# Optimization experiments

Hardware: AMD Instinct MI355X
Metric: run time of the kernel (lower is better)

Reference implementation:

```python
import jax, jax.numpy as jnp
import numpy as np

D_MODEL = 512
N_HEADS = 8
D_KV = 64
EPS = 1e-6
ROPE_THETA = 10000.0


def _rms_norm(x, w):
    # T5-style RMSNorm: no mean subtraction, no bias, variance in fp32.
    var = jnp.mean(x.astype(jnp.float32) ** 2, axis=-1, keepdims=True)
    return (x * jax.lax.rsqrt(var + EPS)).astype(x.dtype) * w


def _rope_cos_sin(pos, dk):
    # pos: [B, T] int -> cos/sin: [B, 1, T, dk]
    inv_freq = 1.0 / (ROPE_THETA ** (jnp.arange(0, dk, 2, dtype=jnp.float32) / dk))
    ang = pos.astype(jnp.float32)[:, :, None] * inv_freq[None, None, :]  # [B,T,dk/2]
    ang = jnp.concatenate([ang, ang], axis=-1)                            # [B,T,dk]
    return jnp.cos(ang)[:, None], jnp.sin(ang)[:, None]


def _rotate_half(x):
    h = x.shape[-1] // 2
    return jnp.concatenate([-x[..., h:], x[..., :h]], axis=-1)


def _mha(x, mask, wq, wk, wv, wo, pos=None):
    # x: [B, T, D]; mask: [B, H, T, T] additive
    B, T, _ = x.shape
    def proj(w):
        return (x @ w).reshape(B, T, N_HEADS, D_KV).transpose(0, 2, 1, 3)  # [B,H,T,dk]
    q, k, v = proj(wq), proj(wk), proj(wv)
    if pos is not None:
        cos, sin = _rope_cos_sin(pos, D_KV)
        cos, sin = cos.astype(x.dtype), sin.astype(x.dtype)
        q = q * cos + _rotate_half(q) * sin
        k = k * cos + _rotate_half(k) * sin
    scale = 1.0 / np.sqrt(D_KV)
    scores = jnp.einsum('bhqd,bhkd->bhqk', q, k) * scale + mask
    attn = jax.nn.softmax(scores.astype(jnp.float32), axis=-1).astype(scores.dtype)
    out = jnp.einsum('bhqk,bhkd->bhqd', attn, v)
    out = out.transpose(0, 2, 1, 3).reshape(B, T, N_HEADS * D_KV)
    return out @ wo


def setup_inputs() -> dict:
    key = jax.random.key(0)
    ks = jax.random.split(key, 12)
    B, T = 8, 1024
    s = 1.0 / np.sqrt(D_MODEL)
    inp = {
        'h': jax.random.normal(ks[0], (B, T, D_MODEL), dtype=jnp.float32),
        'pos': jnp.broadcast_to(jnp.arange(T, dtype=jnp.int64 if jax.config.jax_enable_x64 else jnp.int32)[None, :], (B, T)),
        't_mask': jnp.zeros((B, N_HEADS, T, T), dtype=jnp.float32),
        'g_mask': jnp.zeros((T, N_HEADS, B, B), dtype=jnp.float32),
        'ln_t_w': jnp.ones((D_MODEL,), dtype=jnp.float32),
        'ln_g_w': jnp.ones((D_MODEL,), dtype=jnp.float32),
    }
    names = ['wq_t', 'wk_t', 'wv_t', 'wo_t', 'wq_g', 'wk_g', 'wv_g', 'wo_g']
    for i, n in enumerate(names):
        inp[n] = jax.random.normal(ks[i + 1], (D_MODEL, D_MODEL), dtype=jnp.float32) * s
    return inp


def reference(h, pos, t_mask, g_mask, ln_t_w, ln_g_w,
              wq_t, wk_t, wv_t, wo_t, wq_g, wk_g, wv_g, wo_g):
    # --- time attention (over T axis, with RoPE) ---
    normed = _rms_norm(h, ln_t_w)
    attn_t = _mha(normed, t_mask, wq_t, wk_t, wv_t, wo_t, pos=pos)
    h = h + attn_t  # dropout p=0 (eval)
    # --- group attention (over B axis, no RoPE) ---
    h = h.transpose(1, 0, 2)  # [T, B, D]
    normed = _rms_norm(h, ln_g_w)
    attn_g = _mha(normed, g_mask, wq_g, wk_g, wv_g, wo_g, pos=None)
    h = h + attn_g
    return h.transpose(1, 0, 2)  # back to [B, T, D]
```

## Files before the change

### kernel.cpp

```cpp
#include <hip/hip_runtime.h>
#include <hip/hip_bf16.h>
#include <math.h>


typedef __bf16 bf16x8 __attribute__((ext_vector_type(8)));
typedef __bf16 bf16x4 __attribute__((ext_vector_type(4)));
typedef float  f32x4  __attribute__((ext_vector_type(4)));

#define LN1E4_OVER_32 0.2878231366242558f

__global__ __launch_bounds__(256) void transpose_w(
    const float* w0, const float* w1, const float* w2, const float* w3,
    const float* w4, const float* w5, const float* w6, const float* w7,
    __bf16* qkvT_t, __bf16* oT_t, __bf16* qkvT_g, __bf16* oT_g)
{
    int mat = blockIdx.z;
    const float* src; __bf16* dst; int rowOff;
    switch (mat) {
        case 0: src=w0; dst=qkvT_t; rowOff=0;    break;
        case 1: src=w1; dst=qkvT_t; rowOff=512;  break;
        case 2: src=w2; dst=qkvT_t; rowOff=1024; break;
        case 3: src=w3; dst=oT_t;   rowOff=0;    break;
        case 4: src=w4; dst=qkvT_g; rowOff=0;    break;
        case 5: src=w5; dst=qkvT_g; rowOff=512;  break;
        case 6: src=w6; dst=qkvT_g; rowOff=1024; break;
        default: src=w7; dst=oT_g;  rowOff=0;    break;
    }
    __shared__ float tile[32][33];
    int n0 = blockIdx.x * 32, k0 = blockIdx.y * 32;
    int tt = threadIdx.x;
    int kr = tt >> 3, nc = (tt & 7) * 4;
    float4 v = *(const float4*)(src + (size_t)(k0 + kr) * 512 + n0 + nc);
    tile[kr][nc+0] = v.x; tile[kr][nc+1] = v.y; tile[kr][nc+2] = v.z; tile[kr][nc+3] = v.w;
    __syncthreads();
    int nr = tt >> 3, kc = (tt & 7) * 4;
    bf16x4 o;
    o[0] = (__bf16)tile[kc+0][nr]; o[1] = (__bf16)tile[kc+1][nr];
    o[2] = (__bf16)tile[kc+2][nr]; o[3] = (__bf16)tile[kc+3][nr];
    *(bf16x4*)(dst + (size_t)(rowOff + n0 + nr) * 512 + k0 + kc) = o;
}

__global__ __launch_bounds__(256) void rmsnorm_k(
    const float* __restrict__ x, const float* __restrict__ w,
    __bf16* __restrict__ y, int remap)
{
    int row = blockIdx.x * 4 + (threadIdx.x >> 6);
    int l = threadIdx.x & 63;
    const float* xr = x + (size_t)row * 512 + l * 8;
    float4 a = *(const float4*)xr;
    float4 b = *(const float4*)(xr + 4);
    float ss = a.x*a.x + a.y*a.y + a.z*a.z + a.w*a.w
             + b.x*b.x + b.y*b.y + b.z*b.z + b.w*b.w;
    for (int m = 1; m < 64; m <<= 1) ss += __shfl_xor(ss, m);
    float rms = rsqrtf(ss * (1.0f / 512.0f) + 1e-6f);
    float4 wa = *(const float4*)(w + l * 8);
    float4 wb = *(const float4*)(w + l * 8 + 4);
    int orow = remap ? ((row & 1023) * 8 + (row >> 10)) : row;
    bf16x8 o;
    o[0] = (__bf16)(a.x * rms * wa.x); o[1] = (__bf16)(a.y * rms * wa.y);
    o[2] = (__bf16)(a.z * rms * wa.z); o[3] = (__bf16)(a.w * rms * wa.w);
    o[4] = (__bf16)(b.x * rms * wb.x); o[5] = (__bf16)(b.y * rms * wb.y);
    o[6] = (__bf16)(b.z * rms * wb.z); o[7] = (__bf16)(b.w * rms * wb.w);
    *(bf16x8*)(y + (size_t)orow * 512 + l * 8) = o;
}

__global__ __launch_bounds__(256) void gemm_ep(
    const __bf16* __restrict__ A, const __bf16* __restrict__ Bt,
    const int* __restrict__ pos, const float* __restrict__ resid,
    float* __restrict__ outF,
    __bf16* __restrict__ o0, __bf16* __restrict__ o1, __bf16* __restrict__ o2,
    int mode)
{
    __shared__ __bf16 As[128 * 32];
    __shared__ __bf16 Bs[128 * 32];
    int l = threadIdx.x & 63, w = threadIdx.x >> 6;
    int l16 = l & 15, quad = l >> 4;
    int wm = w >> 1, wn = w & 1;
    int mblk = blockIdx.y * 128, nblk = blockIdx.x * 128;
    f32x4 acc[4][4] = {};

    for (int k0 = 0; k0 < 512; k0 += 32) {
        __syncthreads();
        #pragma unroll
        for (int it = 0; it < 2; ++it) {
            int c = threadIdx.x + it * 256;
            int row = c >> 2, col = (c & 3) << 3;
            *(bf16x8*)(As + c * 8) = *(const bf16x8*)(A  + (size_t)(mblk + row) * 512 + k0 + col);
            *(bf16x8*)(Bs + c * 8) = *(const bf16x8*)(Bt + (size_t)(nblk + row) * 512 + k0 + col);
        }
        __syncthreads();
        bf16x8 aF[4], bF[4];
        #pragma unroll
        for (int mt = 0; mt < 4; mt++) aF[mt] = *(bf16x8*)(As + (wm * 64 + mt * 16 + l16) * 32 + quad * 8);
        #pragma unroll
        for (int nt = 0; nt < 4; nt++) bF[nt] = *(bf16x8*)(Bs + (wn * 64 + nt * 16 + l16) * 32 + quad * 8);
        #pragma unroll
        for (int mt = 0; mt < 4; mt++)
            #pragma unroll
            for (int nt = 0; nt < 4; nt++)
                acc[mt][nt] = __builtin_amdgcn_mfma_f32_16x16x32_bf16(aF[mt], bF[nt], acc[mt][nt], 0, 0, 0);
    }

    int colbase = nblk + wn * 64;
    if (mode == 0 || mode == 2) {
        int mat = colbase >> 9;
        int hh  = (colbase & 511) >> 6;
        __bf16* dst = (mat == 0) ? o0 : (mat == 1) ? o1 : o2;
        bool isQ = (mat == 0), isV = (mat == 2);
        #pragma unroll
        for (int mt = 0; mt < 4; mt++) {
            #pragma unroll
            for (int r = 0; r < 4; r++) {
                int grow = mblk + wm * 64 + mt * 16 + quad * 4 + r;
                if (mode == 0) {
                    int b = grow >> 10, t = grow & 1023;
                    if (!isV) {
                        int p = pos[grow];
                        #pragma unroll
                        for (int nt = 0; nt < 2; nt++) {
                            int i = nt * 16 + l16;
                            float ang = (float)p * __expf((float)i * -LN1E4_OVER_32);
                            float c, s; sincosf(ang, &s, &c);
                            float x1 = acc[mt][nt][r], x2 = acc[mt][nt + 2][r];
                            float y1 = x1 * c - x2 * s;
                            float y2 = x2 * c + x1 * s;
                            if (isQ) { y1 *= 0.125f; y2 *= 0.125f; }
                            size_t base = ((size_t)(b * 8 + hh) * 1024 + t) * 64;
                            dst[base + i]      = (__bf16)y1;
                            dst[base + i + 32] = (__bf16)y2;
                        }
                    } else {
                        #pragma unroll
                        for (int nt = 0; nt < 4; nt++) {
                            int d = nt * 16 + l16;
                            dst[((size_t)(b * 8 + hh) * 64 + d) * 1024 + t] = (__bf16)acc[mt][nt][r];
                        }
                    }
                } else {
                    int t = grow >> 3, b = grow & 7;
                    size_t base = (((size_t)t * 8 + hh) * 8 + b) * 64;
                    #pragma unroll
                    for (int nt = 0; nt < 4; nt++) {
                        float v = acc[mt][nt][r];
                        if (isQ) v *= 0.125f;
                        dst[base + nt * 16 + l16] = (__bf16)v;
                    }
                }
            }
        }
    } else {
        #pragma unroll
        for (int mt = 0; mt < 4; mt++)
            #pragma unroll
            for (int r = 0; r < 4; r++) {
                int grow = mblk + wm * 64 + mt * 16 + quad * 4 + r;
                int orow = (mode == 3) ? (((grow & 7) << 10) + (grow >> 3)) : grow;
                #pragma unroll
                for (int nt = 0; nt < 4; nt++) {
                    int col = colbase + nt * 16 + l16;
                    size_t oi = (size_t)orow * 512 + col;
                    outF[oi] = acc[mt][nt][r] + resid[oi];
                }
            }
    }
}

__global__ __launch_bounds__(256) void flash_t(
    const __bf16* __restrict__ q, const __bf16* __restrict__ k,
    const __bf16* __restrict__ vt, const float* __restrict__ tmask,
    __bf16* __restrict__ ctx)
{
    int bh = blockIdx.y;
    int w = threadIdx.x >> 6, l = threadIdx.x & 63;
    int l16 = l & 15, quad = l >> 4;
    int q0 = blockIdx.x * 64 + w * 16;

    __shared__ __bf16 Ks[64 * 72];
    __shared__ __bf16 Vs[64 * 72];
    __shared__ __bf16 Ps[4][16 * 72];

    bf16x8 aQ0, aQ1;
    {
        const __bf16* qb = q + ((size_t)bh * 1024 + q0 + l16) * 64 + quad * 8;
        aQ0 = *(const bf16x8*)qb;
        aQ1 = *(const bf16x8*)(qb + 32);
    }
    f32x4 o[4] = {};
    float m_i[4], l_i[4];
    #pragma unroll
    for (int r = 0; r < 4; r++) { m_i[r] = -INFINITY; l_i[r] = 0.0f; }

    for (int jb = 0; jb < 1024; jb += 64) {
        __syncthreads();
        #pragma unroll
        for (int it = 0; it < 2; ++it) {
            int c = threadIdx.x + it * 256;
            int row = c >> 3, col = (c & 7) << 3;
            *(bf16x8*)&Ks[row * 72 + col] = *(const bf16x8*)&k [((size_t)bh * 1024 + jb + row) * 64 + col];
            *(bf16x8*)&Vs[row * 72 + col] = *(const bf16x8*)&vt[((size_t)bh * 64 + row) * 1024 + jb + col];
        }
        __syncthreads();

        f32x4 s[4] = {};
        #pragma unroll
        for (int nt = 0; nt < 4; nt++) {
            bf16x8 b0 = *(bf16x8*)&Ks[(nt * 16 + l16) * 72 + quad * 8];
            bf16x8 b1 = *(bf16x8*)&Ks[(nt * 16 + l16) * 72 + 32 + quad * 8];
            s[nt] = __builtin_amdgcn_mfma_f32_16x16x32_bf16(aQ0, b0, s[nt], 0, 0, 0);
            s[nt] = __builtin_amdgcn_mfma_f32_16x16x32_bf16(aQ1, b1, s[nt], 0, 0, 0);
        }
        const float* mr = tmask + (size_t)bh * 1024 * 1024 + (size_t)(q0 + quad * 4) * 1024 + jb + l16;
        #pragma unroll
        for (int r = 0; r < 4; r++)
            #pragma unroll
            for (int nt = 0; nt < 4; nt++)
                s[nt][r] += mr[(size_t)r * 1024 + nt * 16];

        float alpha[4];
        #pragma unroll
        for (int r = 0; r < 4; r++) {
            float mx = fmaxf(fmaxf(s[0][r], s[1][r]), fmaxf(s[2][r], s[3][r]));
            mx = fmaxf(mx, __shfl_xor(mx, 1));
            mx = fmaxf(mx, __shfl_xor(mx, 2));
            mx = fmaxf(mx, __shfl_xor(mx, 4));
            mx = fmaxf(mx, __shfl_xor(mx, 8));
            float mn = fmaxf(m_i[r], mx);
            alpha[r] = __expf(m_i[r] - mn);
            m_i[r] = mn;
            float rs = 0.0f;
            #pragma unroll
            for (int nt = 0; nt < 4; nt++) {
                float p = __expf(s[nt][r] - mn);
                s[nt][r] = p;
                rs += p;
            }
            rs += __shfl_xor(rs, 1);
            rs += __shfl_xor(rs, 2);
            rs += __shfl_xor(rs, 4);
            rs += __shfl_xor(rs, 8);
            l_i[r] = l_i[r] * alpha[r] + rs;
        }
        #pragma unroll
        for (int dt = 0; dt < 4; dt++)
            #pragma unroll
            for (int r = 0; r < 4; r++) o[dt][r] *= alpha[r];

        __bf16* ps = Ps[w];
        #pragma unroll
        for (int nt = 0; nt < 4; nt++)
            #pragma unroll
            for (int r = 0; r < 4; r++)
                ps[(quad * 4 + r) * 72 + nt * 16 + l16] = (__bf16)s[nt][r];
        bf16x8 aP0 = *(bf16x8*)&ps[l16 * 72 + quad * 8];
        bf16x8 aP1 = *(bf16x8*)&ps[l16 * 72 + 32 + quad * 8];
        #pragma unroll
        for (int dt = 0; dt < 4; dt++) {
            bf16x8 bv0 = *(bf16x8*)&Vs[(dt * 16 + l16) * 72 + quad * 8];
            bf16x8 bv1 = *(bf16x8*)&Vs[(dt * 16 + l16) * 72 + 32 + quad * 8];
            o[dt] = __builtin_amdgcn_mfma_f32_16x16x32_bf16(aP0, bv0, o[dt], 0, 0, 0);
            o[dt] = __builtin_amdgcn_mfma_f32_16x16x32_bf16(aP1, bv1, o[dt], 0, 0, 0);
        }
    }

    int b = bh >> 3, h = bh & 7;
    #pragma unroll
    for (int dt = 0; dt < 4; dt++)
        #pragma unroll
        for (int r = 0; r < 4; r++) {
            float v = o[dt][r] / l_i[r];
            ctx[((size_t)b * 1024 + q0 + quad * 4 + r) * 512 + h * 64 + dt * 16 + l16] = (__bf16)v;
        }
}

__global__ __launch_bounds__(256) void group_attn(
    const __bf16* __restrict__ qg, const __bf16* __restrict__ kg,
    const __bf16* __restrict__ vg, const float* __restrict__ gmask,
    __bf16* __restrict__ ctxg)
{
    int tid = blockIdx.x * 256 + threadIdx.x;
    int t = tid >> 6, h = (tid >> 3) & 7, bq = tid & 7;
    size_t base = ((size_t)t * 8 + h) * 512;

    float qv[64];
    #pragma unroll
    for (int d0 = 0; d0 < 64; d0 += 8) {
        bf16x8 qq = *(const bf16x8*)&qg[base + (size_t)bq * 64 + d0];
        #pragma unroll
        for (int u = 0; u < 8; u++) qv[d0 + u] = (float)qq[u];
    }
    float s[8];
    #pragma unroll
    for (int j = 0; j < 8; j++) {
        float acc = 0.0f;
        #pragma unroll
        for (int d0 = 0; d0 < 64; d0 += 8) {
            bf16x8 kk = *(const bf16x8*)&kg[base + (size_t)j * 64 + d0];
            #pragma unroll
            for (int u = 0; u < 8; u++) acc += qv[d0 + u] * (float)kk[u];
        }
        s[j] = acc + gmask[(((size_t)t * 8 + h) * 8 + bq) * 8 + j];
    }
    float mx = s[0];
    #pragma unroll
    for (int j = 1; j < 8; j++) mx = fmaxf(mx, s[j]);
    float sum = 0.0f;
    #pragma unroll
    for (int j = 0; j < 8; j++) { s[j] = __expf(s[j] - mx); sum += s[j]; }
    float inv = 1.0f / sum;

    #pragma unroll
    for (int d0 = 0; d0 < 64; d0 += 8) {
        float o8[8] = {};
        #pragma unroll
        for (int j = 0; j < 8; j++) {
            bf16x8 vv = *(const bf16x8*)&vg[base + (size_t)j * 64 + d0];
            float pj = s[j];
            #pragma unroll
            for (int u = 0; u < 8; u++) o8[u] += pj * (float)vv[u];
        }
        bf16x8 ob;
        #pragma unroll
        for (int u = 0; u < 8; u++) ob[u] = (__bf16)(o8[u] * inv);
        *(bf16x8*)&ctxg[((size_t)t * 8 + bq) * 512 + h * 64 + d0] = ob;
    }
}

extern "C" void kernel_launch(void* const* d_in, const int* in_sizes, int n_in,
                              void* d_out, int out_size, void* d_ws, size_t ws_size,
                              hipStream_t stream)
{
    const float* h      = (const float*)d_in[0];
    const int*   pos    = (const int*)  d_in[1];
    const float* t_mask = (const float*)d_in[2];
    const float* g_mask = (const float*)d_in[3];
    const float* ln_t_w = (const float*)d_in[4];
    const float* ln_g_w = (const float*)d_in[5];
    const float* wq_t = (const float*)d_in[6];
    const float* wk_t = (const float*)d_in[7];
    const float* wv_t = (const float*)d_in[8];
    const float* wo_t = (const float*)d_in[9];
    const float* wq_g = (const float*)d_in[10];
    const float* wk_g = (const float*)d_in[11];
    const float* wv_g = (const float*)d_in[12];
    const float* wo_g = (const float*)d_in[13];
    float* out = (float*)d_out;

    char* ws = (char*)d_ws;
    const size_t MB = 1ull << 20;
    __bf16* qkvT_t = (__bf16*)ws;
    __bf16* oT_t   = qkvT_t + 786432;
    __bf16* qkvT_g = qkvT_t + 1048576;
    __bf16* oT_g   = qkvT_t + 1835008;
    __bf16* normed = (__bf16*)(ws + 4 * MB);
    __bf16* qb     = (__bf16*)(ws + 12 * MB);
    __bf16* kb     = (__bf16*)(ws + 20 * MB);
    __bf16* vb     = (__bf16*)(ws + 28 * MB);
    __bf16* ctx    = (__bf16*)(ws + 36 * MB);
    float*  h2     = (float*) (ws + 44 * MB);

    transpose_w<<<dim3(16, 16, 8), 256, 0, stream>>>(
        wq_t, wk_t, wv_t, wo_t, wq_g, wk_g, wv_g, wo_g,
        qkvT_t, oT_t, qkvT_g, oT_g);

    rmsnorm_k<<<2048, 256, 0, stream>>>(h, ln_t_w, normed, 0);
    gemm_ep<<<dim3(12, 64), 256, 0, stream>>>(normed, qkvT_t, pos, nullptr, nullptr,
                                              qb, kb, vb, 0);
    flash_t<<<dim3(16, 64), 256, 0, stream>>>(qb, kb, vb, t_mask, ctx);
    gemm_ep<<<dim3(4, 64), 256, 0, stream>>>(ctx, oT_t, nullptr, h, h2,
                                             nullptr, nullptr, nullptr, 1);

    rmsnorm_k<<<2048, 256, 0, stream>>>(h2, ln_g_w, normed, 1);
    gemm_ep<<<dim3(12, 64), 256, 0, stream>>>(normed, qkvT_g, nullptr, nullptr, nullptr,
                                              qb, kb, vb, 2);
    group_attn<<<256, 256, 0, stream>>>(qb, kb, vb, g_mask, ctx);
    gemm_ep<<<dim3(4, 64), 256, 0, stream>>>(ctx, oT_g, nullptr, h2, out,
                                             nullptr, nullptr, nullptr, 3);
}
```

Measured before the change: 564.9 us.

## Use direct global-to-LDS loads in GEMM and stage V-transpose stores via LDS

The GEMM tile loads now use the global_load_lds builtin, so data goes straight into shared memory without passing through registers. The V-projection epilogue, which wrote transposed scalar bf16 values with a large stride, now stages each 16-row tile in shared memory and writes 16-byte vectors along the T dimension. RoPE sincosf is also replaced by the faster intrinsic __sincosf, trading some accuracy for large angles (positions up to 1023). A barrier is added before the epilogue so the staging area can reuse the GEMM shared buffer.

```diff
diff --git a/kernel.cpp b/kernel.cpp
--- a/kernel.cpp
+++ b/kernel.cpp
@@ -8,6 +8,12 @@
 typedef float  f32x4  __attribute__((ext_vector_type(4)));
 
 #define LN1E4_OVER_32 0.2878231366242558f
+
+__device__ __forceinline__ void gld16(const void* g, void* l) {
+    __builtin_amdgcn_global_load_lds((const __attribute__((address_space(1))) void*)g,
+                                     (__attribute__((address_space(3))) void*)l,
+                                     16, 0, 0);
+}
 
 __global__ __launch_bounds__(256) void transpose_w(
     const float* w0, const float* w1, const float* w2, const float* w3,
@@ -71,9 +77,11 @@
     __bf16* __restrict__ o0, __bf16* __restrict__ o1, __bf16* __restrict__ o2,
     int mode)
 {
-    __shared__ __bf16 As[128 * 32];
-    __shared__ __bf16 Bs[128 * 32];
-    int l = threadIdx.x & 63, w = threadIdx.x >> 6;
+    __shared__ __bf16 smem[8192];
+    __bf16* As = smem;
+    __bf16* Bs = smem + 4096;
+    int tid = threadIdx.x;
+    int l = tid & 63, w = tid >> 6;
     int l16 = l & 15, quad = l >> 4;
     int wm = w >> 1, wn = w & 1;
     int mblk = blockIdx.y * 128, nblk = blockIdx.x * 128;
@@ -82,11 +90,11 @@
     for (int k0 = 0; k0 < 512; k0 += 32) {
         __syncthreads();
         #pragma unroll
-        for (int it = 0; it < 2; ++it) {
-            int c = threadIdx.x + it * 256;
-            int row = c >> 2, col = (c & 3) << 3;
-            *(bf16x8*)(As + c * 8) = *(const bf16x8*)(A  + (size_t)(mblk + row) * 512 + k0 + col);
-            *(bf16x8*)(Bs + c * 8) = *(const bf16x8*)(Bt + (size_t)(nblk + row) * 512 + k0 + col);
+        for (int i = 0; i < 2; ++i) {
+            int idx = i * 256 + tid;
+            int row = idx >> 2, c8 = (idx & 3) * 8;
+            gld16(A  + (size_t)(mblk + row) * 512 + k0 + c8, (char*)As + (size_t)idx * 16);
+            gld16(Bt + (size_t)(nblk + row) * 512 + k0 + c8, (char*)Bs + (size_t)idx * 16);
         }
         __syncthreads();
         bf16x8 aF[4], bF[4];
@@ -100,6 +108,7 @@
             for (int nt = 0; nt < 4; nt++)
                 acc[mt][nt] = __builtin_amdgcn_mfma_f32_16x16x32_bf16(aF[mt], bF[nt], acc[mt][nt], 0, 0, 0);
     }
+    __syncthreads();
 
     int colbase = nblk + wn * 64;
     if (mode == 0 || mode == 2) {
@@ -107,20 +116,39 @@
         int hh  = (colbase & 511) >> 6;
         __bf16* dst = (mat == 0) ? o0 : (mat == 1) ? o1 : o2;
         bool isQ = (mat == 0), isV = (mat == 2);
-        #pragma unroll
-        for (int mt = 0; mt < 4; mt++) {
-            #pragma unroll
-            for (int r = 0; r < 4; r++) {
-                int grow = mblk + wm * 64 + mt * 16 + quad * 4 + r;
-                if (mode == 0) {
-                    int b = grow >> 10, t = grow & 1023;
-                    if (!isV) {
+        if (mode == 0 && isV) {
+            __bf16* vls = smem + (size_t)w * 1536;
+            #pragma unroll
+            for (int mt = 0; mt < 4; mt++) {
+                #pragma unroll
+                for (int nt = 0; nt < 4; nt++)
+                    #pragma unroll
+                    for (int r = 0; r < 4; r++)
+                        vls[(nt * 16 + l16) * 24 + quad * 4 + r] = (__bf16)acc[mt][nt][r];
+                int grow0 = mblk + wm * 64 + mt * 16;
+                int b = grow0 >> 10, t0 = grow0 & 1023;
+                #pragma unroll
+                for (int i = 0; i < 2; ++i) {
+                    int li = i * 64 + l;
+                    int d = li >> 1, t8 = (li & 1) * 8;
+                    bf16x8 vv = *(bf16x8*)&vls[d * 24 + t8];
+                    *(bf16x8*)&dst[((size_t)(b * 8 + hh) * 64 + d) * 1024 + t0 + t8] = vv;
+                }
+            }
+        } else {
+            #pragma unroll
+            for (int mt = 0; mt < 4; mt++) {
+                #pragma unroll
+                for (int r = 0; r < 4; r++) {
+                    int grow = mblk + wm * 64 + mt * 16 + quad * 4 + r;
+                    if (mode == 0) {
+                        int b = grow >> 10, t = grow & 1023;
                         int p = pos[grow];
                         #pragma unroll
                         for (int nt = 0; nt < 2; nt++) {
                             int i = nt * 16 + l16;
                             float ang = (float)p * __expf((float)i * -LN1E4_OVER_32);
-                            float c, s; sincosf(ang, &s, &c);
+                            float c, s; __sincosf(ang, &s, &c);
                             float x1 = acc[mt][nt][r], x2 = acc[mt][nt + 2][r];
                             float y1 = x1 * c - x2 * s;
                             float y2 = x2 * c + x1 * s;
@@ -130,20 +158,14 @@
                             dst[base + i + 32] = (__bf16)y2;
                         }
                     } else {
+                        int t = grow >> 3, b = grow & 7;
+                        size_t base = (((size_t)t * 8 + hh) * 8 + b) * 64;
                         #pragma unroll
                         for (int nt = 0; nt < 4; nt++) {
-                            int d = nt * 16 + l16;
-                            dst[((size_t)(b * 8 + hh) * 64 + d) * 1024 + t] = (__bf16)acc[mt][nt][r];
+                            float v = acc[mt][nt][r];
+                            if (isQ) v *= 0.125f;
+                            dst[base + nt * 16 + l16] = (__bf16)v;
                         }
-                    }
-                } else {
-                    int t = grow >> 3, b = grow & 7;
-                    size_t base = (((size_t)t * 8 + hh) * 8 + b) * 64;
-                    #pragma unroll
-                    for (int nt = 0; nt < 4; nt++) {
-                        float v = acc[mt][nt][r];
-                        if (isQ) v *= 0.125f;
-                        dst[base + nt * 16 + l16] = (__bf16)v;
                     }
                 }
             }
```

After: 542.2 us. -4.0%, faster.
